# Kernel optimization log

Hardware: AMD Instinct MI355X
Metric: run time of the kernel (lower is better)

Reference implementation:

```python
import jax, jax.numpy as jnp
import numpy as np

B, C, T, H = 32, 256, 512, 8
EPS = 1e-5
NEG_INF = jnp.float32(-1e9)


def setup_inputs() -> dict:
    key = jax.random.key(0)
    ks = jax.random.split(key, 10)
    inp = {
        "seq": jax.random.normal(ks[0], (B, C, T), dtype=jnp.float32),
        "mask": jax.random.randint(ks[1], (B, T), 0, 2, dtype=jnp.int32),
        "Wq": jax.random.normal(ks[2], (C, C), dtype=jnp.float32) * 0.05,
        "bq": jnp.zeros((C,), dtype=jnp.float32),
        "Wk": jax.random.normal(ks[3], (C, C), dtype=jnp.float32) * 0.05,
        "bk": jnp.zeros((C,), dtype=jnp.float32),
        "Wv": jax.random.normal(ks[4], (C, C), dtype=jnp.float32) * 0.05,
        "bv": jnp.zeros((C,), dtype=jnp.float32),
        "gamma": jnp.ones((C,), dtype=jnp.float32),
        "beta": jnp.zeros((C,), dtype=jnp.float32),
    }
    return inp


def reference(seq, mask, Wq, bq, Wk, bk, Wv, bv, gamma, beta):
    d = C // H  # per-head dim
    s = jnp.transpose(seq, (0, 2, 1))  # [B, T, C]
    # ReLU'd projections (torch Linear: x @ W.T + b)
    Q = jax.nn.relu(s @ Wq.T + bq)
    K = jax.nn.relu(s @ Wk.T + bk)
    V = jax.nn.relu(s @ Wv.T + bv)
    # head split: channel block h -> head h (torch cat(split, dim=0) order = h*B+b)
    Qh = Q.reshape(B, T, H, d).transpose(2, 0, 1, 3)  # [H, B, T, d]
    Kh = K.reshape(B, T, H, d).transpose(2, 0, 1, 3)
    Vh = V.reshape(B, T, H, d).transpose(2, 0, 1, 3)
    scores = jnp.einsum('hbtd,hbsd->hbts', Qh, Kh) / jnp.sqrt(jnp.float32(d))
    # additive key mask before softmax
    key_mask = (mask == 0)[None, :, None, :]  # [1, B, 1, T]
    scores = jnp.where(key_mask, NEG_INF, scores)
    # multiplicative query mask after softmax
    qmask = mask.astype(jnp.float32)[None, :, :, None]  # [1, B, T, 1]
    att = jax.nn.softmax(scores, axis=-1) * qmask
    # dropout with keep_prob=1.0 is identity
    o = jnp.einsum('hbts,hbsd->hbtd', att, Vh)  # [H, B, T, d]
    x = o.transpose(1, 2, 0, 3).reshape(B, T, C)  # heads concatenated on channels
    x = jnp.transpose(x, (0, 2, 1))  # [B, C, T]
    # BatchNorm(pre_mask=True, post_mask=is_mask=True), training-mode batch stats
    m = (mask == 1)[:, None, :]  # [B, 1, T]
    x = jnp.where(m, x, jnp.float32(0.0))
    mean = jnp.mean(x, axis=(0, 2))
    var = jnp.mean((x - mean[None, :, None]) ** 2, axis=(0, 2))  # biased var (torch BN)
    xn = (x - mean[None, :, None]) * jax.lax.rsqrt(var + EPS)[None, :, None]
    x = gamma[None, :, None] * xn + beta[None, :, None]
    x = jnp.where(m, x, jnp.float32(0.0))
    return x
```

## Files before the change

kernel.cpp:

```cpp
#include <hip/hip_runtime.h>
#include <math.h>

#define NB 32
#define NC 256
#define NT 512
#define NH 8
#define ND 32
#define SCALE 0.17677669529663687f
#define LOG2E 1.4426950408889634f
#define QSCALE (SCALE * LOG2E)
#define MASKVAL (-1.4426950408889634e9f)

typedef __attribute__((ext_vector_type(8))) __bf16 bf16x8;
typedef __attribute__((ext_vector_type(4))) __bf16 bf16x4;
typedef __attribute__((ext_vector_type(4))) float  f32x4;

static __device__ __forceinline__ f32x4 mfma16x16x32(bf16x8 a, bf16x8 b, f32x4 c) {
    return __builtin_amdgcn_mfma_f32_16x16x32_bf16(a, b, c, 0, 0, 0);
}

__global__ __launch_bounds__(256) void qkv_mfma(
    const float* __restrict__ seq,
    const float* __restrict__ Wq, const float* __restrict__ bq,
    const float* __restrict__ Wk, const float* __restrict__ bk,
    const float* __restrict__ Wv, const float* __restrict__ bv,
    __bf16* __restrict__ Qh, __bf16* __restrict__ Kh, __bf16* __restrict__ Vh,
    float* __restrict__ stats)
{
    __shared__ __bf16 As[64][264];
    __shared__ __bf16 Ws[3][64][40];

    const int tid = threadIdx.x;
    const int t0  = blockIdx.x * 64;
    const int co0 = blockIdx.y * 64;
    const int bb  = blockIdx.z;

    if (blockIdx.x == 0 && blockIdx.y == 0 && bb == 0 && tid < 128)
        ((float4*)stats)[tid] = make_float4(0.f, 0.f, 0.f, 0.f);

    {
        const int cl = tid & 15;
        const int t4 = (tid >> 4) * 4;
        for (int it = 0; it < 16; ++it) {
            const int c = it*16 + cl;
            const float4 v = *(const float4*)&seq[((size_t)(bb*NC + c))*NT + t0 + t4];
            As[t4+0][c] = (__bf16)v.x;
            As[t4+1][c] = (__bf16)v.y;
            As[t4+2][c] = (__bf16)v.z;
            As[t4+3][c] = (__bf16)v.w;
        }
    }

    const float* Wp[3] = {Wq, Wk, Wv};

    f32x4 acc[3][4];
    #pragma unroll
    for (int p = 0; p < 3; ++p)
        #pragma unroll
        for (int n = 0; n < 4; ++n) acc[p][n] = (f32x4)0.f;

    const int l   = tid & 63;
    const int w   = tid >> 6;
    const int lr  = l & 15;
    const int lk8 = (l >> 4) * 8;

    int wp_[6], wco[6], wc4[6];
    #pragma unroll
    for (int i = 0; i < 6; ++i) {
        const int lin = i*256 + tid;
        wp_[i] = lin >> 9;
        const int r = lin & 511;
        wco[i] = r >> 3;
        wc4[i] = (r & 7) * 4;
    }

    float4 wreg[6];
    #pragma unroll
    for (int i = 0; i < 6; ++i)
        wreg[i] = *(const float4*)&Wp[wp_[i]][(size_t)(co0 + wco[i])*NC + wc4[i]];

    for (int kc = 0; kc < 8; ++kc) {
        __syncthreads();
        #pragma unroll
        for (int i = 0; i < 6; ++i) {
            bf16x4 wb;
            wb[0] = (__bf16)wreg[i].x; wb[1] = (__bf16)wreg[i].y;
            wb[2] = (__bf16)wreg[i].z; wb[3] = (__bf16)wreg[i].w;
            *(bf16x4*)&Ws[wp_[i]][wco[i]][wc4[i]] = wb;
        }
        __syncthreads();

        if (kc < 7) {
            #pragma unroll
            for (int i = 0; i < 6; ++i)
                wreg[i] = *(const float4*)&Wp[wp_[i]][(size_t)(co0 + wco[i])*NC + (kc+1)*32 + wc4[i]];
        }

        const bf16x8 a = *(const bf16x8*)&As[w*16 + lr][kc*32 + lk8];
        #pragma unroll
        for (int p = 0; p < 3; ++p)
            #pragma unroll
            for (int n = 0; n < 4; ++n) {
                const bf16x8 bfr = *(const bf16x8*)&Ws[p][n*16 + lr][lk8];
                acc[p][n] = mfma16x16x32(a, bfr, acc[p][n]);
            }
    }

    const float* bias[3] = {bq, bk, bv};
    __bf16* outp[3] = {Qh, Kh, Vh};
    #pragma unroll
    for (int p = 0; p < 3; ++p) {
        #pragma unroll
        for (int n = 0; n < 4; ++n) {
            const int c  = co0 + n*16 + lr;
            const int hh = c >> 5, jj = c & 31;
            const float bv_ = bias[p][c];
            const float sc  = (p == 0) ? QSCALE : 1.f;
            __bf16* op = outp[p] + ((size_t)(bb*NH + hh)*NT)*ND + jj;
            #pragma unroll
            for (int r = 0; r < 4; ++r) {
                const int t = t0 + w*16 + (l>>4)*4 + r;
                op[(size_t)t*ND] = (__bf16)(fmaxf(acc[p][n][r] + bv_, 0.f) * sc);
            }
        }
    }
}

__global__ __launch_bounds__(256) void attn_mfma(
    const __bf16* __restrict__ Qh, const __bf16* __restrict__ Kh,
    const __bf16* __restrict__ Vh, const int* __restrict__ mask,
    float* __restrict__ xout, float* __restrict__ stats)
{
    __shared__ __bf16 Ks[64][40];
    __shared__ __bf16 VTs[32][72];
    __shared__ __bf16 PA[128][72];
    __shared__ float  bnsum[32][4];
    __shared__ float  bnsum2[32][4];

    const int tid = threadIdx.x;
    const int t0  = blockIdx.x * 128;
    const int h   = blockIdx.y;
    const int bb  = blockIdx.z;
    const int bh  = bb*NH + h;
    const __bf16* Qp = Qh + (size_t)bh*NT*ND;
    const __bf16* Kp = Kh + (size_t)bh*NT*ND;
    const __bf16* Vp = Vh + (size_t)bh*NT*ND;

    const int l   = tid & 63;
    const int w   = tid >> 6;
    const int lr  = l & 15;
    const int g   = l >> 4;
    const int lk8 = g * 8;

    bf16x8 qb[2];
    #pragma unroll
    for (int ct = 0; ct < 2; ++ct)
        qb[ct] = *(const bf16x8*)&Qp[(size_t)(t0 + w*32 + ct*16 + lr)*ND + lk8];

    f32x4 accO[2][2];
    #pragma unroll
    for (int jt = 0; jt < 2; ++jt)
        #pragma unroll
        for (int ct = 0; ct < 2; ++ct) accO[jt][ct] = (f32x4)0.f;
    float m_run[2] = {-1e30f, -1e30f};
    float l_run[2] = {0.f, 0.f};

    const int kv_s = tid >> 2, kv_c8 = (tid & 3) * 8;

    for (int s0 = 0; s0 < NT; s0 += 64) {
        const uint4 kreg = *(const uint4*)&Kp[(size_t)(s0 + kv_s)*ND + kv_c8];
        ushort4 vreg[2];
        #pragma unroll
        for (int it = 0; it < 2; ++it) {
            const int lin = it*256 + tid;
            const int s = lin >> 3, j4 = (lin & 7) * 4;
            vreg[it] = *(const ushort4*)&Vp[(size_t)(s0 + s)*ND + j4];
        }
        const unsigned long long mw = __ballot(mask[bb*NT + s0 + l] != 0);

        __syncthreads();
        *(uint4*)&Ks[kv_s][kv_c8] = kreg;
        #pragma unroll
        for (int it = 0; it < 2; ++it) {
            const int lin = it*256 + tid;
            const int s = lin >> 3, j4 = (lin & 7) * 4;
            const __bf16* vb = (const __bf16*)&vreg[it];
            VTs[j4+0][s] = vb[0]; VTs[j4+1][s] = vb[1];
            VTs[j4+2][s] = vb[2]; VTs[j4+3][s] = vb[3];
        }
        __syncthreads();

        bf16x8 kA[4];
        #pragma unroll
        for (int st = 0; st < 4; ++st)
            kA[st] = *(const bf16x8*)&Ks[st*16 + lr][lk8];

        #pragma unroll
        for (int ct = 0; ct < 2; ++ct) {
            f32x4 sst[4];
            #pragma unroll
            for (int st = 0; st < 4; ++st)
                sst[st] = mfma16x16x32(kA[st], qb[ct], (f32x4)0.f);

            float v[16];
            float mx = -1e30f;
            #pragma unroll
            for (int st = 0; st < 4; ++st)
                #pragma unroll
                for (int r = 0; r < 4; ++r) {
                    const int s = st*16 + g*4 + r;
                    const float val = ((mw >> s) & 1ull) ? sst[st][r] : MASKVAL;
                    v[st*4+r] = val;
                    mx = fmaxf(mx, val);
                }
            mx = fmaxf(mx, __shfl_xor(mx, 16));
            mx = fmaxf(mx, __shfl_xor(mx, 32));
            const float m_new = fmaxf(m_run[ct], mx);
            const float f = exp2f(m_run[ct] - m_new);

            const int trow = w*32 + ct*16 + lr;
            float ssum = 0.f;
            #pragma unroll
            for (int st = 0; st < 4; ++st) {
                bf16x4 pb4;
                #pragma unroll
                for (int r = 0; r < 4; ++r) {
                    const float p = exp2f(v[st*4+r] - m_new);
                    ssum += p;
                    pb4[r] = (__bf16)p;
                }
                *(bf16x4*)&PA[trow][st*16 + g*4] = pb4;
            }
            ssum += __shfl_xor(ssum, 16);
            ssum += __shfl_xor(ssum, 32);
            l_run[ct] = l_run[ct]*f + ssum;
            m_run[ct] = m_new;

            #pragma unroll
            for (int jt = 0; jt < 2; ++jt)
                #pragma unroll
                for (int r = 0; r < 4; ++r)
                    accO[jt][ct][r] *= f;
        }

        #pragma unroll
        for (int kh = 0; kh < 2; ++kh) {
            bf16x8 va[2], pb[2];
            #pragma unroll
            for (int jt = 0; jt < 2; ++jt)
                va[jt] = *(const bf16x8*)&VTs[jt*16 + lr][kh*32 + lk8];
            #pragma unroll
            for (int ct = 0; ct < 2; ++ct)
                pb[ct] = *(const bf16x8*)&PA[w*32 + ct*16 + lr][kh*32 + lk8];
            #pragma unroll
            for (int jt = 0; jt < 2; ++jt)
                #pragma unroll
                for (int ct = 0; ct < 2; ++ct)
                    accO[jt][ct] = mfma16x16x32(va[jt], pb[ct], accO[jt][ct]);
        }
    }

    float psum[2][4], psq[2][4];
    #pragma unroll
    for (int jt = 0; jt < 2; ++jt)
        #pragma unroll
        for (int r = 0; r < 4; ++r) { psum[jt][r] = 0.f; psq[jt][r] = 0.f; }

    #pragma unroll
    for (int ct = 0; ct < 2; ++ct) {
        const int t = t0 + w*32 + ct*16 + lr;
        const float rl = mask[bb*NT + t] ? (1.f / l_run[ct]) : 0.f;
        #pragma unroll
        for (int jt = 0; jt < 2; ++jt) {
            #pragma unroll
            for (int r = 0; r < 4; ++r) {
                const int c = h*ND + jt*16 + g*4 + r;
                const float o = accO[jt][ct][r] * rl;
                xout[((size_t)(bb*NC + c))*NT + t] = o;
                psum[jt][r] += o;
                psq[jt][r]  += o*o;
            }
        }
    }
    #pragma unroll
    for (int jt = 0; jt < 2; ++jt)
        #pragma unroll
        for (int r = 0; r < 4; ++r) {
            #pragma unroll
            for (int off = 1; off < 16; off <<= 1) {
                psum[jt][r] += __shfl_xor(psum[jt][r], off);
                psq[jt][r]  += __shfl_xor(psq[jt][r],  off);
            }
        }
    if (lr == 0) {
        #pragma unroll
        for (int jt = 0; jt < 2; ++jt)
            #pragma unroll
            for (int r = 0; r < 4; ++r) {
                bnsum [jt*16 + g*4 + r][w] = psum[jt][r];
                bnsum2[jt*16 + g*4 + r][w] = psq[jt][r];
            }
    }
    __syncthreads();
    if (tid < 32) {
        const float s  = bnsum [tid][0] + bnsum [tid][1] + bnsum [tid][2] + bnsum [tid][3];
        const float s2 = bnsum2[tid][0] + bnsum2[tid][1] + bnsum2[tid][2] + bnsum2[tid][3];
        atomicAdd(&stats[h*ND + tid], s);
        atomicAdd(&stats[NC + h*ND + tid], s2);
    }
}

__global__ __launch_bounds__(256) void bn_apply_kernel(
    float* __restrict__ x, const float* __restrict__ stats,
    const float* __restrict__ gamma, const float* __restrict__ beta,
    const int* __restrict__ mask)
{
    const int idx = blockIdx.x*256 + threadIdx.x;
    const int t4 = idx & 127;
    const int c  = (idx >> 7) & 255;
    const int bb = idx >> 15;
    float4 v = ((const float4*)x)[idx];
    const int4 mk = *(const int4*)&mask[bb*NT + t4*4];
    const float mean = stats[c] * (1.f/16384.f);
    const float var  = fmaxf(stats[NC + c]*(1.f/16384.f) - mean*mean, 0.f);
    const float rstd = rsqrtf(var + 1e-5f);
    const float g = gamma[c], be = beta[c];
    v.x = mk.x ? fmaf((v.x - mean)*rstd, g, be) : 0.f;
    v.y = mk.y ? fmaf((v.y - mean)*rstd, g, be) : 0.f;
    v.z = mk.z ? fmaf((v.z - mean)*rstd, g, be) : 0.f;
    v.w = mk.w ? fmaf((v.w - mean)*rstd, g, be) : 0.f;
    ((float4*)x)[idx] = v;
}

extern "C" void kernel_launch(void* const* d_in, const int* in_sizes, int n_in,
                              void* d_out, int out_size, void* d_ws, size_t ws_size,
                              hipStream_t stream)
{
    const float* seq   = (const float*)d_in[0];
    const int*   mask  = (const int*)  d_in[1];
    const float* Wq    = (const float*)d_in[2];
    const float* bq    = (const float*)d_in[3];
    const float* Wk    = (const float*)d_in[4];
    const float* bk    = (const float*)d_in[5];
    const float* Wv    = (const float*)d_in[6];
    const float* bv    = (const float*)d_in[7];
    const float* gamma = (const float*)d_in[8];
    const float* beta  = (const float*)d_in[9];
    float* out = (float*)d_out;

    const size_t perMat = (size_t)NB*NH*NT*ND;
    __bf16* Qh = (__bf16*)d_ws;
    __bf16* Kh = Qh + perMat;
    __bf16* Vh = Kh + perMat;
    float* stats = (float*)(Vh + perMat);

    qkv_mfma<<<dim3(NT/64, NC/64, NB), 256, 0, stream>>>(
        seq, Wq, bq, Wk, bk, Wv, bv, Qh, Kh, Vh, stats);
    attn_mfma<<<dim3(NT/128, NH, NB), 256, 0, stream>>>(
        Qh, Kh, Vh, mask, out, stats);
    bn_apply_kernel<<<dim3((NB*NC*NT/4)/256), 256, 0, stream>>>(
        out, stats, gamma, beta, mask);
}
```

Before: 156.2 us.

## Restructure attention kernel: 8 waves, K in registers, prefetch, swizzled LDS, lazy rescale

The attention kernel now runs 512 threads with one 16-row query tile per wave instead of two. K tiles are loaded straight from global memory into registers, and K, V and the mask for the next tile are prefetched during the current iteration. The Ks shared buffer is removed, and the V transpose and P buffers use an XOR swizzle in place of padding to avoid LDS bank conflicts. The online softmax skips rescaling unless the running max rises past a threshold, which trims exp and multiply work but lets exponents grow up to 2^8 before renormalisation. More waves per block may raise register pressure and lower occupancy.

Result: slower. 161.3 us (+3.3%).

```diff
diff --git a/kernel.cpp b/kernel.cpp
--- a/kernel.cpp
+++ b/kernel.cpp
@@ -10,6 +10,7 @@
 #define LOG2E 1.4426950408889634f
 #define QSCALE (SCALE * LOG2E)
 #define MASKVAL (-1.4426950408889634e9f)
+#define DEFER_THR 8.0f
 
 typedef __attribute__((ext_vector_type(8))) __bf16 bf16x8;
 typedef __attribute__((ext_vector_type(4))) __bf16 bf16x4;
@@ -126,16 +127,15 @@
     }
 }
 
-__global__ __launch_bounds__(256) void attn_mfma(
+__global__ __launch_bounds__(512) void attn_mfma(
     const __bf16* __restrict__ Qh, const __bf16* __restrict__ Kh,
     const __bf16* __restrict__ Vh, const int* __restrict__ mask,
     float* __restrict__ xout, float* __restrict__ stats)
 {
-    __shared__ __bf16 Ks[64][40];
-    __shared__ __bf16 VTs[32][72];
-    __shared__ __bf16 PA[128][72];
-    __shared__ float  bnsum[32][4];
-    __shared__ float  bnsum2[32][4];
+    __shared__ __bf16 VTs[32*64];
+    __shared__ __bf16 PA[128*64];
+    __shared__ float  bnsum[32][8];
+    __shared__ float  bnsum2[32][8];
 
     const int tid = threadIdx.x;
     const int t0  = blockIdx.x * 128;
@@ -150,148 +150,128 @@
     const int w   = tid >> 6;
     const int lr  = l & 15;
     const int g   = l >> 4;
-    const int lk8 = g * 8;
-
-    bf16x8 qb[2];
-    #pragma unroll
-    for (int ct = 0; ct < 2; ++ct)
-        qb[ct] = *(const bf16x8*)&Qp[(size_t)(t0 + w*32 + ct*16 + lr)*ND + lk8];
-
-    f32x4 accO[2][2];
-    #pragma unroll
-    for (int jt = 0; jt < 2; ++jt)
-        #pragma unroll
-        for (int ct = 0; ct < 2; ++ct) accO[jt][ct] = (f32x4)0.f;
-    float m_run[2] = {-1e30f, -1e30f};
-    float l_run[2] = {0.f, 0.f};
-
-    const int kv_s = tid >> 2, kv_c8 = (tid & 3) * 8;
+    const int swz = (lr & 7) << 3;
+
+    const bf16x8 qb = *(const bf16x8*)&Qp[(size_t)(t0 + w*16 + lr)*ND + g*8];
+
+    f32x4 accO[2];
+    accO[0] = (f32x4)0.f; accO[1] = (f32x4)0.f;
+    float m_run = -1e30f, l_run = 0.f;
+
+    const int v_s = tid >> 3, v_j4 = (tid & 7) * 4;
+
+    ushort4 vreg = *(const ushort4*)&Vp[(size_t)v_s*ND + v_j4];
+    bf16x8 kA[4];
+    #pragma unroll
+    for (int st = 0; st < 4; ++st)
+        kA[st] = *(const bf16x8*)&Kp[(size_t)(st*16 + lr)*ND + g*8];
+    unsigned long long mw = __ballot(mask[bb*NT + l] != 0);
 
     for (int s0 = 0; s0 < NT; s0 += 64) {
-        const uint4 kreg = *(const uint4*)&Kp[(size_t)(s0 + kv_s)*ND + kv_c8];
-        ushort4 vreg[2];
-        #pragma unroll
-        for (int it = 0; it < 2; ++it) {
-            const int lin = it*256 + tid;
-            const int s = lin >> 3, j4 = (lin & 7) * 4;
-            vreg[it] = *(const ushort4*)&Vp[(size_t)(s0 + s)*ND + j4];
-        }
-        const unsigned long long mw = __ballot(mask[bb*NT + s0 + l] != 0);
-
         __syncthreads();
-        *(uint4*)&Ks[kv_s][kv_c8] = kreg;
-        #pragma unroll
-        for (int it = 0; it < 2; ++it) {
-            const int lin = it*256 + tid;
-            const int s = lin >> 3, j4 = (lin & 7) * 4;
-            const __bf16* vb = (const __bf16*)&vreg[it];
-            VTs[j4+0][s] = vb[0]; VTs[j4+1][s] = vb[1];
-            VTs[j4+2][s] = vb[2]; VTs[j4+3][s] = vb[3];
+        {
+            const __bf16* vb = (const __bf16*)&vreg;
+            #pragma unroll
+            for (int kk = 0; kk < 4; ++kk) {
+                const int j = v_j4 + kk;
+                VTs[j*64 + (v_s ^ ((j & 7) << 3))] = vb[kk];
+            }
         }
         __syncthreads();
 
-        bf16x8 kA[4];
+        const unsigned long long mwc = mw;
+        bf16x8 kAc[4];
+        #pragma unroll
+        for (int st = 0; st < 4; ++st) kAc[st] = kA[st];
+        if (s0 + 64 < NT) {
+            const int sn = s0 + 64;
+            vreg = *(const ushort4*)&Vp[(size_t)(sn + v_s)*ND + v_j4];
+            #pragma unroll
+            for (int st = 0; st < 4; ++st)
+                kA[st] = *(const bf16x8*)&Kp[(size_t)(sn + st*16 + lr)*ND + g*8];
+            mw = __ballot(mask[bb*NT + sn + l] != 0);
+        }
+
+        f32x4 sst[4];
         #pragma unroll
         for (int st = 0; st < 4; ++st)
-            kA[st] = *(const bf16x8*)&Ks[st*16 + lr][lk8];
-
-        #pragma unroll
-        for (int ct = 0; ct < 2; ++ct) {
-            f32x4 sst[4];
-            #pragma unroll
-            for (int st = 0; st < 4; ++st)
-                sst[st] = mfma16x16x32(kA[st], qb[ct], (f32x4)0.f);
-
-            float v[16];
-            float mx = -1e30f;
-            #pragma unroll
-            for (int st = 0; st < 4; ++st)
-                #pragma unroll
-                for (int r = 0; r < 4; ++r) {
-                    const int s = st*16 + g*4 + r;
-                    const float val = ((mw >> s) & 1ull) ? sst[st][r] : MASKVAL;
-                    v[st*4+r] = val;
-                    mx = fmaxf(mx, val);
-                }
-            mx = fmaxf(mx, __shfl_xor(mx, 16));
-            mx = fmaxf(mx, __shfl_xor(mx, 32));
-            const float m_new = fmaxf(m_run[ct], mx);
-            const float f = exp2f(m_run[ct] - m_new);
-
-            const int trow = w*32 + ct*16 + lr;
-            float ssum = 0.f;
-            #pragma unroll
-            for (int st = 0; st < 4; ++st) {
-                bf16x4 pb4;
-                #pragma unroll
-                for (int r = 0; r < 4; ++r) {
-                    const float p = exp2f(v[st*4+r] - m_new);
-                    ssum += p;
-                    pb4[r] = (__bf16)p;
-                }
-                *(bf16x4*)&PA[trow][st*16 + g*4] = pb4;
-            }
-            ssum += __shfl_xor(ssum, 16);
-            ssum += __shfl_xor(ssum, 32);
-            l_run[ct] = l_run[ct]*f + ssum;
-            m_run[ct] = m_new;
-
+            sst[st] = mfma16x16x32(kAc[st], qb, (f32x4)0.f);
+
+        float v[16];
+        float mx = -1e30f;
+        #pragma unroll
+        for (int st = 0; st < 4; ++st)
+            #pragma unroll
+            for (int r = 0; r < 4; ++r) {
+                const int s = st*16 + g*4 + r;
+                const float val = ((mwc >> s) & 1ull) ? sst[st][r] : MASKVAL;
+                v[st*4+r] = val;
+                mx = fmaxf(mx, val);
+            }
+        mx = fmaxf(mx, __shfl_xor(mx, 16));
+        mx = fmaxf(mx, __shfl_xor(mx, 32));
+
+        if (!__all(mx <= m_run + DEFER_THR)) {
+            const float m_new = fmaxf(m_run, mx);
+            const float f = exp2f(m_run - m_new);
+            l_run *= f;
             #pragma unroll
             for (int jt = 0; jt < 2; ++jt)
                 #pragma unroll
-                for (int r = 0; r < 4; ++r)
-                    accO[jt][ct][r] *= f;
-        }
+                for (int r = 0; r < 4; ++r) accO[jt][r] *= f;
+            m_run = m_new;
+        }
+
+        float ssum = 0.f;
+        #pragma unroll
+        for (int st = 0; st < 4; ++st) {
+            bf16x4 pb4;
+            #pragma unroll
+            for (int r = 0; r < 4; ++r) {
+                const float p = exp2f(v[st*4+r] - m_run);
+                ssum += p;
+                pb4[r] = (__bf16)p;
+            }
+            *(bf16x4*)&PA[(w*16 + lr)*64 + ((st*16 + g*4) ^ swz)] = pb4;
+        }
+        ssum += __shfl_xor(ssum, 16);
+        ssum += __shfl_xor(ssum, 32);
+        l_run += ssum;
 
         #pragma unroll
         for (int kh = 0; kh < 2; ++kh) {
-            bf16x8 va[2], pb[2];
-            #pragma unroll
-            for (int jt = 0; jt < 2; ++jt)
-                va[jt] = *(const bf16x8*)&VTs[jt*16 + lr][kh*32 + lk8];
-            #pragma unroll
-            for (int ct = 0; ct < 2; ++ct)
-                pb[ct] = *(const bf16x8*)&PA[w*32 + ct*16 + lr][kh*32 + lk8];
-            #pragma unroll
-            for (int jt = 0; jt < 2; ++jt)
-                #pragma unroll
-                for (int ct = 0; ct < 2; ++ct)
-                    accO[jt][ct] = mfma16x16x32(va[jt], pb[ct], accO[jt][ct]);
-        }
-    }
-
+            const bf16x8 pb = *(const bf16x8*)&PA[(w*16 + lr)*64 + ((kh*32 + g*8) ^ swz)];
+            #pragma unroll
+            for (int jt = 0; jt < 2; ++jt) {
+                const bf16x8 va = *(const bf16x8*)&VTs[(jt*16 + lr)*64 + ((kh*32 + g*8) ^ swz)];
+                accO[jt] = mfma16x16x32(va, pb, accO[jt]);
+            }
+        }
+    }
+
+    const int t = t0 + w*16 + lr;
+    const float rl = mask[bb*NT + t] ? (1.f / l_run) : 0.f;
     float psum[2][4], psq[2][4];
     #pragma unroll
+    for (int jt = 0; jt < 2; ++jt) {
+        #pragma unroll
+        for (int r = 0; r < 4; ++r) {
+            const int c = h*ND + jt*16 + g*4 + r;
+            const float o = accO[jt][r] * rl;
+            xout[((size_t)(bb*NC + c))*NT + t] = o;
+            psum[jt][r] = o;
+            psq[jt][r]  = o*o;
+        }
+    }
+    #pragma unroll
     for (int jt = 0; jt < 2; ++jt)
         #pragma unroll
-        for (int r = 0; r < 4; ++r) { psum[jt][r] = 0.f; psq[jt][r] = 0.f; }
-
-    #pragma unroll
-    for (int ct = 0; ct < 2; ++ct) {
-        const int t = t0 + w*32 + ct*16 + lr;
-        const float rl = mask[bb*NT + t] ? (1.f / l_run[ct]) : 0.f;
-        #pragma unroll
-        for (int jt = 0; jt < 2; ++jt) {
-            #pragma unroll
-            for (int r = 0; r < 4; ++r) {
-                const int c = h*ND + jt*16 + g*4 + r;
-                const float o = accO[jt][ct][r] * rl;
-                xout[((size_t)(bb*NC + c))*NT + t] = o;
-                psum[jt][r] += o;
-                psq[jt][r]  += o*o;
-            }
-        }
-    }
-    #pragma unroll
-    for (int jt = 0; jt < 2; ++jt)
-        #pragma unroll
-        for (int r = 0; r < 4; ++r) {
+        for (int r = 0; r < 4; ++r)
             #pragma unroll
             for (int off = 1; off < 16; off <<= 1) {
                 psum[jt][r] += __shfl_xor(psum[jt][r], off);
                 psq[jt][r]  += __shfl_xor(psq[jt][r],  off);
             }
-        }
     if (lr == 0) {
         #pragma unroll
         for (int jt = 0; jt < 2; ++jt)
@@ -303,8 +283,9 @@
     }
     __syncthreads();
     if (tid < 32) {
-        const float s  = bnsum [tid][0] + bnsum [tid][1] + bnsum [tid][2] + bnsum [tid][3];
-        const float s2 = bnsum2[tid][0] + bnsum2[tid][1] + bnsum2[tid][2] + bnsum2[tid][3];
+        float s = 0.f, s2 = 0.f;
+        #pragma unroll
+        for (int ww = 0; ww < 8; ++ww) { s += bnsum[tid][ww]; s2 += bnsum2[tid][ww]; }
         atomicAdd(&stats[h*ND + tid], s);
         atomicAdd(&stats[NC + h*ND + tid], s2);
     }
@@ -356,7 +337,7 @@
 
     qkv_mfma<<<dim3(NT/64, NC/64, NB), 256, 0, stream>>>(
         seq, Wq, bq, Wk, bk, Wv, bv, Qh, Kh, Vh, stats);
-    attn_mfma<<<dim3(NT/128, NH, NB), 256, 0, stream>>>(
+    attn_mfma<<<dim3(NT/128, NH, NB), 512, 0, stream>>>(
         Qh, Kh, Vh, mask, out, stats);
     bn_apply_kernel<<<dim3((NB*NC*NT/4)/256), 256, 0, stream>>>(
         out, stats, gamma, beta, mask);
```

## Fold key mask into V, compute softmax denominator via MFMA, defer rescaling

Applied to the files above, without the earlier changes.

The QKV kernel now multiplies V by the key mask and writes it transposed, so the attention kernel drops the per-score mask select and loads V rows directly. The softmax row sum is accumulated by an extra MFMA against a mask row stored in LDS, and the running-max rescale is skipped unless the max grows past a threshold. The change also adds XOR-swizzled LDS layouts for V and P, register prefetch of the next K/V tile, and s_setprio around the MFMA sections. The intent is to cut VALU and shuffle work in the inner loop and avoid LDS bank conflicts. The risks are overflow from deferred rescaling and a change in numerics, since masked keys now enter the max and exponentials before V zeroes them.

Result: faster. 147.5 us (-5.6%).

```diff
diff --git a/kernel.cpp b/kernel.cpp
--- a/kernel.cpp
+++ b/kernel.cpp
@@ -9,7 +9,7 @@
 #define SCALE 0.17677669529663687f
 #define LOG2E 1.4426950408889634f
 #define QSCALE (SCALE * LOG2E)
-#define MASKVAL (-1.4426950408889634e9f)
+#define DEFER_THR 8.0f
 
 typedef __attribute__((ext_vector_type(8))) __bf16 bf16x8;
 typedef __attribute__((ext_vector_type(4))) __bf16 bf16x4;
@@ -20,11 +20,11 @@
 }
 
 __global__ __launch_bounds__(256) void qkv_mfma(
-    const float* __restrict__ seq,
+    const float* __restrict__ seq, const int* __restrict__ mask,
     const float* __restrict__ Wq, const float* __restrict__ bq,
     const float* __restrict__ Wk, const float* __restrict__ bk,
     const float* __restrict__ Wv, const float* __restrict__ bv,
-    __bf16* __restrict__ Qh, __bf16* __restrict__ Kh, __bf16* __restrict__ Vh,
+    __bf16* __restrict__ Qh, __bf16* __restrict__ Kh, __bf16* __restrict__ VhT,
     float* __restrict__ stats)
 {
     __shared__ __bf16 As[64][264];
@@ -106,34 +106,54 @@
             }
     }
 
-    const float* bias[3] = {bq, bk, bv};
-    __bf16* outp[3] = {Qh, Kh, Vh};
-    #pragma unroll
-    for (int p = 0; p < 3; ++p) {
+    const int tba = t0 + w*16 + (l>>4)*4;
+
+    {
+        const float* bias2[2] = {bq, bk};
+        __bf16* outp2[2] = {Qh, Kh};
+        #pragma unroll
+        for (int p = 0; p < 2; ++p) {
+            #pragma unroll
+            for (int n = 0; n < 4; ++n) {
+                const int c  = co0 + n*16 + lr;
+                const int hh = c >> 5, jj = c & 31;
+                const float bv_ = bias2[p][c];
+                const float sc  = (p == 0) ? QSCALE : 1.f;
+                __bf16* op = outp2[p] + ((size_t)(bb*NH + hh)*NT)*ND + jj;
+                #pragma unroll
+                for (int r = 0; r < 4; ++r)
+                    op[(size_t)(tba + r)*ND] = (__bf16)(fmaxf(acc[p][n][r] + bv_, 0.f) * sc);
+            }
+        }
+    }
+
+    {
+        float km[4];
+        #pragma unroll
+        for (int r = 0; r < 4; ++r)
+            km[r] = (mask[bb*NT + tba + r] != 0) ? 1.f : 0.f;
         #pragma unroll
         for (int n = 0; n < 4; ++n) {
             const int c  = co0 + n*16 + lr;
             const int hh = c >> 5, jj = c & 31;
-            const float bv_ = bias[p][c];
-            const float sc  = (p == 0) ? QSCALE : 1.f;
-            __bf16* op = outp[p] + ((size_t)(bb*NH + hh)*NT)*ND + jj;
-            #pragma unroll
-            for (int r = 0; r < 4; ++r) {
-                const int t = t0 + w*16 + (l>>4)*4 + r;
-                op[(size_t)t*ND] = (__bf16)(fmaxf(acc[p][n][r] + bv_, 0.f) * sc);
-            }
+            const float bv_ = bv[c];
+            bf16x4 vv;
+            #pragma unroll
+            for (int r = 0; r < 4; ++r)
+                vv[r] = (__bf16)(fmaxf(acc[2][n][r] + bv_, 0.f) * km[r]);
+            *(bf16x4*)&VhT[((size_t)(bb*NH + hh)*ND + jj)*NT + tba] = vv;
         }
     }
 }
 
 __global__ __launch_bounds__(256) void attn_mfma(
     const __bf16* __restrict__ Qh, const __bf16* __restrict__ Kh,
-    const __bf16* __restrict__ Vh, const int* __restrict__ mask,
+    const __bf16* __restrict__ VhT, const int* __restrict__ mask,
     float* __restrict__ xout, float* __restrict__ stats)
 {
     __shared__ __bf16 Ks[64][40];
-    __shared__ __bf16 VTs[32][72];
-    __shared__ __bf16 PA[128][72];
+    __shared__ __bf16 VTs[33*64];
+    __shared__ __bf16 PA[128*64];
     __shared__ float  bnsum[32][4];
     __shared__ float  bnsum2[32][4];
 
@@ -142,122 +162,119 @@
     const int h   = blockIdx.y;
     const int bb  = blockIdx.z;
     const int bh  = bb*NH + h;
-    const __bf16* Qp = Qh + (size_t)bh*NT*ND;
-    const __bf16* Kp = Kh + (size_t)bh*NT*ND;
-    const __bf16* Vp = Vh + (size_t)bh*NT*ND;
+    const __bf16* Qp = Qh  + (size_t)bh*NT*ND;
+    const __bf16* Kp = Kh  + (size_t)bh*NT*ND;
+    const __bf16* Vp = VhT + (size_t)bh*ND*NT;
 
     const int l   = tid & 63;
     const int w   = tid >> 6;
     const int lr  = l & 15;
     const int g   = l >> 4;
-    const int lk8 = g * 8;
+    const int swz = (lr & 7) << 3;
 
     bf16x8 qb[2];
     #pragma unroll
     for (int ct = 0; ct < 2; ++ct)
-        qb[ct] = *(const bf16x8*)&Qp[(size_t)(t0 + w*32 + ct*16 + lr)*ND + lk8];
+        qb[ct] = *(const bf16x8*)&Qp[(size_t)(t0 + w*32 + ct*16 + lr)*ND + g*8];
 
     f32x4 accO[2][2];
+    f32x4 accL[2];
     #pragma unroll
     for (int jt = 0; jt < 2; ++jt)
         #pragma unroll
         for (int ct = 0; ct < 2; ++ct) accO[jt][ct] = (f32x4)0.f;
+    accL[0] = (f32x4)0.f; accL[1] = (f32x4)0.f;
     float m_run[2] = {-1e30f, -1e30f};
-    float l_run[2] = {0.f, 0.f};
 
     const int kv_s = tid >> 2, kv_c8 = (tid & 3) * 8;
+    const int vt_j = tid >> 3, vt_s8 = (tid & 7) * 8;
+
+    uint4 kreg = *(const uint4*)&Kp[(size_t)kv_s*ND + kv_c8];
+    uint4 vreg = *(const uint4*)&Vp[(size_t)vt_j*NT + vt_s8];
+    int   mreg = (tid < 64) ? mask[bb*NT + tid] : 0;
 
     for (int s0 = 0; s0 < NT; s0 += 64) {
-        const uint4 kreg = *(const uint4*)&Kp[(size_t)(s0 + kv_s)*ND + kv_c8];
-        ushort4 vreg[2];
-        #pragma unroll
-        for (int it = 0; it < 2; ++it) {
-            const int lin = it*256 + tid;
-            const int s = lin >> 3, j4 = (lin & 7) * 4;
-            vreg[it] = *(const ushort4*)&Vp[(size_t)(s0 + s)*ND + j4];
-        }
-        const unsigned long long mw = __ballot(mask[bb*NT + s0 + l] != 0);
-
         __syncthreads();
         *(uint4*)&Ks[kv_s][kv_c8] = kreg;
-        #pragma unroll
-        for (int it = 0; it < 2; ++it) {
-            const int lin = it*256 + tid;
-            const int s = lin >> 3, j4 = (lin & 7) * 4;
-            const __bf16* vb = (const __bf16*)&vreg[it];
-            VTs[j4+0][s] = vb[0]; VTs[j4+1][s] = vb[1];
-            VTs[j4+2][s] = vb[2]; VTs[j4+3][s] = vb[3];
-        }
+        *(uint4*)&VTs[vt_j*64 + (vt_s8 ^ ((vt_j & 7) << 3))] = vreg;
+        if (tid < 64) VTs[32*64 + tid] = (__bf16)(mreg ? 1.f : 0.f);
         __syncthreads();
 
+        if (s0 + 64 < NT) {
+            const int sn = s0 + 64;
+            kreg = *(const uint4*)&Kp[(size_t)(sn + kv_s)*ND + kv_c8];
+            vreg = *(const uint4*)&Vp[(size_t)vt_j*NT + sn + vt_s8];
+            if (tid < 64) mreg = mask[bb*NT + sn + tid];
+        }
+
         bf16x8 kA[4];
         #pragma unroll
         for (int st = 0; st < 4; ++st)
-            kA[st] = *(const bf16x8*)&Ks[st*16 + lr][lk8];
+            kA[st] = *(const bf16x8*)&Ks[st*16 + lr][g*8];
+        f32x4 sst[2][4];
+        __builtin_amdgcn_s_setprio(1);
+        #pragma unroll
+        for (int ct = 0; ct < 2; ++ct)
+            #pragma unroll
+            for (int st = 0; st < 4; ++st)
+                sst[ct][st] = mfma16x16x32(kA[st], qb[ct], (f32x4)0.f);
+        __builtin_amdgcn_s_setprio(0);
 
         #pragma unroll
         for (int ct = 0; ct < 2; ++ct) {
-            f32x4 sst[4];
+            float mx = -1e30f;
             #pragma unroll
             for (int st = 0; st < 4; ++st)
-                sst[st] = mfma16x16x32(kA[st], qb[ct], (f32x4)0.f);
-
-            float v[16];
-            float mx = -1e30f;
-            #pragma unroll
-            for (int st = 0; st < 4; ++st)
-                #pragma unroll
-                for (int r = 0; r < 4; ++r) {
-                    const int s = st*16 + g*4 + r;
-                    const float val = ((mw >> s) & 1ull) ? sst[st][r] : MASKVAL;
-                    v[st*4+r] = val;
-                    mx = fmaxf(mx, val);
-                }
+                #pragma unroll
+                for (int r = 0; r < 4; ++r) mx = fmaxf(mx, sst[ct][st][r]);
             mx = fmaxf(mx, __shfl_xor(mx, 16));
             mx = fmaxf(mx, __shfl_xor(mx, 32));
-            const float m_new = fmaxf(m_run[ct], mx);
-            const float f = exp2f(m_run[ct] - m_new);
+
+            if (!__all(mx <= m_run[ct] + DEFER_THR)) {
+                const float m_new = fmaxf(m_run[ct], mx);
+                const float f = exp2f(m_run[ct] - m_new);
+                #pragma unroll
+                for (int jt = 0; jt < 2; ++jt)
+                    #pragma unroll
+                    for (int r = 0; r < 4; ++r) accO[jt][ct][r] *= f;
+                #pragma unroll
+                for (int r = 0; r < 4; ++r) accL[ct][r] *= f;
+                m_run[ct] = m_new;
+            }
 
             const int trow = w*32 + ct*16 + lr;
-            float ssum = 0.f;
             #pragma unroll
             for (int st = 0; st < 4; ++st) {
                 bf16x4 pb4;
                 #pragma unroll
-                for (int r = 0; r < 4; ++r) {
-                    const float p = exp2f(v[st*4+r] - m_new);
-                    ssum += p;
-                    pb4[r] = (__bf16)p;
-                }
-                *(bf16x4*)&PA[trow][st*16 + g*4] = pb4;
-            }
-            ssum += __shfl_xor(ssum, 16);
-            ssum += __shfl_xor(ssum, 32);
-            l_run[ct] = l_run[ct]*f + ssum;
-            m_run[ct] = m_new;
-
+                for (int r = 0; r < 4; ++r)
+                    pb4[r] = (__bf16)exp2f(sst[ct][st][r] - m_run[ct]);
+                *(bf16x4*)&PA[trow*64 + ((st*16 + g*4) ^ swz)] = pb4;
+            }
+        }
+
+        __builtin_amdgcn_s_setprio(1);
+        #pragma unroll
+        for (int kh = 0; kh < 2; ++kh) {
+            const int co = (kh*32 + g*8);
+            bf16x8 va[2], pb[2];
             #pragma unroll
             for (int jt = 0; jt < 2; ++jt)
-                #pragma unroll
-                for (int r = 0; r < 4; ++r)
-                    accO[jt][ct][r] *= f;
-        }
-
-        #pragma unroll
-        for (int kh = 0; kh < 2; ++kh) {
-            bf16x8 va[2], pb[2];
-            #pragma unroll
-            for (int jt = 0; jt < 2; ++jt)
-                va[jt] = *(const bf16x8*)&VTs[jt*16 + lr][kh*32 + lk8];
+                va[jt] = *(const bf16x8*)&VTs[(jt*16 + lr)*64 + (co ^ swz)];
+            const bf16x8 vam = *(const bf16x8*)&VTs[32*64 + co];
             #pragma unroll
             for (int ct = 0; ct < 2; ++ct)
-                pb[ct] = *(const bf16x8*)&PA[w*32 + ct*16 + lr][kh*32 + lk8];
+                pb[ct] = *(const bf16x8*)&PA[(w*32 + ct*16 + lr)*64 + (co ^ swz)];
             #pragma unroll
             for (int jt = 0; jt < 2; ++jt)
                 #pragma unroll
                 for (int ct = 0; ct < 2; ++ct)
                     accO[jt][ct] = mfma16x16x32(va[jt], pb[ct], accO[jt][ct]);
-        }
+            #pragma unroll
+            for (int ct = 0; ct < 2; ++ct)
+                accL[ct] = mfma16x16x32(vam, pb[ct], accL[ct]);
+        }
+        __builtin_amdgcn_s_setprio(0);
     }
 
     float psum[2][4], psq[2][4];
@@ -269,7 +286,7 @@
     #pragma unroll
     for (int ct = 0; ct < 2; ++ct) {
         const int t = t0 + w*32 + ct*16 + lr;
-        const float rl = mask[bb*NT + t] ? (1.f / l_run[ct]) : 0.f;
+        const float rl = mask[bb*NT + t] ? (1.f / accL[ct][0]) : 0.f;
         #pragma unroll
         for (int jt = 0; jt < 2; ++jt) {
             #pragma unroll
@@ -285,13 +302,12 @@
     #pragma unroll
     for (int jt = 0; jt < 2; ++jt)
         #pragma unroll
-        for (int r = 0; r < 4; ++r) {
+        for (int r = 0; r < 4; ++r)
             #pragma unroll
             for (int off = 1; off < 16; off <<= 1) {
                 psum[jt][r] += __shfl_xor(psum[jt][r], off);
                 psq[jt][r]  += __shfl_xor(psq[jt][r],  off);
             }
-        }
     if (lr == 0) {
         #pragma unroll
         for (int jt = 0; jt < 2; ++jt)
@@ -349,15 +365,15 @@
     float* out = (float*)d_out;
 
     const size_t perMat = (size_t)NB*NH*NT*ND;
-    __bf16* Qh = (__bf16*)d_ws;
-    __bf16* Kh = Qh + perMat;
-    __bf16* Vh = Kh + perMat;
-    float* stats = (float*)(Vh + perMat);
+    __bf16* Qh  = (__bf16*)d_ws;
+    __bf16* Kh  = Qh + perMat;
+    __bf16* VhT = Kh + perMat;
+    float* stats = (float*)(VhT + perMat);
 
     qkv_mfma<<<dim3(NT/64, NC/64, NB), 256, 0, stream>>>(
-        seq, Wq, bq, Wk, bk, Wv, bv, Qh, Kh, Vh, stats);
+        seq, mask, Wq, bq, Wk, bk, Wv, bv, Qh, Kh, VhT, stats);
     attn_mfma<<<dim3(NT/128, NH, NB), 256, 0, stream>>>(
-        Qh, Kh, Vh, mask, out, stats);
+        Qh, Kh, VhT, mask, out, stats);
     bn_apply_kernel<<<dim3((NB*NC*NT/4)/256), 256, 0, stream>>>(
         out, stats, gamma, beta, mask);
 }
```
